# Performance work log

Measured on AMD Instinct MI355X. Metric: run time of the kernel, lower is better.

Reference implementation:

```python
import jax, jax.numpy as jnp
import numpy as np

N = 4096      # nodes (= attention seq_len)
D = 256       # dim_h
H = 4         # num_heads
HD = D // H   # head dim
E = 131072    # edges (avg degree 32)


def _ln(x, g, b, eps=1e-5):
    mu = jnp.mean(x, -1, keepdims=True)
    var = jnp.var(x, -1, keepdims=True)
    return (x - mu) * jax.lax.rsqrt(var + eps) * g + b


def setup_inputs() -> dict:
    key = jax.random.key(0)
    ks = jax.random.split(key, 10)
    s = 0.02
    nrm = lambda k, shape: jax.random.normal(k, shape, jnp.float32) * s
    return dict(
        x=jax.random.normal(ks[0], (N, D), jnp.float32),
        edge_index=jax.random.randint(ks[1], (2, E), 0, N, dtype=jnp.int32),
        W_gcn=nrm(ks[2], (D, D)), b_gcn=jnp.zeros((D,), jnp.float32),
        w_qkv=nrm(ks[3], (D, 3 * D)), b_qkv=jnp.zeros((3 * D,), jnp.float32),
        w_out=nrm(ks[4], (D, D)), b_out=jnp.zeros((D,), jnp.float32),
        g1l=jnp.ones((D,), jnp.float32), beta1l=jnp.zeros((D,), jnp.float32),
        g1a=jnp.ones((D,), jnp.float32), beta1a=jnp.zeros((D,), jnp.float32),
        W1=nrm(ks[5], (D, 2 * D)), bf1=jnp.zeros((2 * D,), jnp.float32),
        W2=nrm(ks[6], (2 * D, D)), bf2=jnp.zeros((D,), jnp.float32),
        g2=jnp.ones((D,), jnp.float32), beta2=jnp.zeros((D,), jnp.float32),
    )


def reference(x, edge_index, W_gcn, b_gcn, w_qkv, b_qkv, w_out, b_out,
              g1l, beta1l, g1a, beta1a, W1, bf1, W2, bf2, g2, beta2):
    n = x.shape[0]
    # --- GCNConv: sym-normalized aggregation with self loops ---
    loop = jnp.arange(n, dtype=edge_index.dtype)
    src = jnp.concatenate([edge_index[0], loop])
    dst = jnp.concatenate([edge_index[1], loop])
    deg = jax.ops.segment_sum(jnp.ones_like(src, x.dtype), dst, num_segments=n)
    dinv = jax.lax.rsqrt(deg)  # deg >= 1 thanks to self loops
    h = x @ W_gcn                                  # [N, D]
    msg = h[src] * (dinv[src] * dinv[dst])[:, None]  # gather + edge norm
    x_local = jax.ops.segment_sum(msg, dst, num_segments=n) + b_gcn
    x = _ln(x + x_local, g1l, beta1l)
    # --- Multi-head self-attention over all nodes (one sequence) ---
    qkv = x @ w_qkv + b_qkv
    q, k, v = jnp.split(qkv, 3, axis=-1)
    q = q.reshape(n, H, HD)
    k = k.reshape(n, H, HD)
    v = v.reshape(n, H, HD)
    scale = 1.0 / (HD ** 0.5)
    scores = jnp.einsum('nhd,mhd->hnm', q, k) * scale   # [H, N, N]
    attn = jax.nn.softmax(scores, axis=-1)
    x_attn = jnp.einsum('hnm,mhd->nhd', attn, v).reshape(n, D) @ w_out + b_out
    x = _ln(x + x_attn, g1a, beta1a)
    # --- FFN (D -> 2D -> D, ReLU) ---
    x_ffn = jax.nn.relu(x @ W1 + bf1) @ W2 + bf2
    return _ln(x + x_ffn, g2, beta2)
```

## Files before the change

### kernel.cpp

```cpp
#include <hip/hip_runtime.h>

typedef unsigned short u16;
typedef __bf16 bf16x8 __attribute__((ext_vector_type(8)));
typedef float f32x4 __attribute__((ext_vector_type(4)));

__device__ __forceinline__ u16 f2u(float f) {
    unsigned u = __builtin_bit_cast(unsigned, f);
    return (u16)((u + 0x7FFFu + ((u >> 16) & 1u)) >> 16);
}

__device__ __forceinline__ float u2f(u16 h) {
    return __builtin_bit_cast(float, (unsigned)h << 16);
}

__device__ __forceinline__ void glds16(const u16* g, u16* l) {
    __builtin_amdgcn_global_load_lds((const __attribute__((address_space(1))) unsigned int*)g,
                                     (__attribute__((address_space(3))) unsigned int*)l, 16, 0, 0);
}


__global__ __launch_bounds__(256) void prep_k(
    const float* __restrict__ w0, const float* __restrict__ w1, const float* __restrict__ w2,
    const float* __restrict__ w3, const float* __restrict__ w4, const float* __restrict__ x,
    u16* __restrict__ o0, u16* __restrict__ o1, u16* __restrict__ o2,
    u16* __restrict__ o3, u16* __restrict__ o4, u16* __restrict__ xo,
    int* __restrict__ cnt, int xblocks, int nn) {
    int b = blockIdx.x, t = threadIdx.x;
    if (b < 144) {
        const float* in; u16* out; int R, C, tb;
        if (b < 16)       { in = w0; out = o0; R = 256; C = 256; tb = b; }
        else if (b < 64)  { in = w1; out = o1; R = 256; C = 768; tb = b - 16; }
        else if (b < 80)  { in = w2; out = o2; R = 256; C = 256; tb = b - 64; }
        else if (b < 112) { in = w3; out = o3; R = 256; C = 512; tb = b - 80; }
        else              { in = w4; out = o4; R = 512; C = 256; tb = b - 112; }
        int tcols = C >> 6;
        int tr = tb / tcols, tc = tb - tr * tcols;
        __shared__ float T[64][65];
        int i0 = t >> 6, j = t & 63;
#pragma unroll
        for (int p = 0; p < 16; p++) {
            int r = p * 4 + i0;
            T[r][j] = in[(long)(tr * 64 + r) * C + tc * 64 + j];
        }
        __syncthreads();
#pragma unroll
        for (int p = 0; p < 16; p++) {
            int c = p * 4 + i0;
            out[(long)(tc * 64 + c) * R + tr * 64 + j] = f2u(T[j][c]);
        }
    } else if (b < 144 + xblocks) {
        long base = (long)(b - 144) * 4096;
#pragma unroll
        for (int p = 0; p < 4; p++) {
            long idx = base + p * 1024 + t * 4;
            float4 v = *(const float4*)&x[idx];
            unsigned lo = (unsigned)f2u(v.x) | ((unsigned)f2u(v.y) << 16);
            unsigned hi = (unsigned)f2u(v.z) | ((unsigned)f2u(v.w) << 16);
            *(uint2*)&xo[idx] = uint2{lo, hi};
        }
    } else {
        int i = (b - 144 - xblocks) * 256 + t;
        if (i < nn) cnt[i] = 0;
    }
}


__device__ __forceinline__ void block_ln_stats(float v, float& mu, float& rstd) {
    float s1 = v, s2 = v * v;
#pragma unroll
    for (int m = 1; m < 64; m <<= 1) { s1 += __shfl_xor(s1, m, 64); s2 += __shfl_xor(s2, m, 64); }
    __shared__ float r1[4], r2[4];
    int lane = threadIdx.x & 63, w = threadIdx.x >> 6;
    if (lane == 0) { r1[w] = s1; r2[w] = s2; }
    __syncthreads();
    s1 = r1[0] + r1[1] + r1[2] + r1[3];
    s2 = r2[0] + r2[1] + r2[2] + r2[3];
    mu = s1 * (1.0f / 256.0f);
    float var = s2 * (1.0f / 256.0f) - mu * mu;
    rstd = rsqrtf(var + 1e-5f);
}

__global__ __launch_bounds__(256) void ln_k(const float* __restrict__ a, const float* __restrict__ b,
                                            const float* __restrict__ g, const float* __restrict__ be,
                                            float* __restrict__ out, u16* __restrict__ outbf) {
    int n = blockIdx.x, d = threadIdx.x;
    long i = (long)n * 256 + d;
    float v = a[i] + b[i];
    float mu, rs;
    block_ln_stats(v, mu, rs);
    float y = (v - mu) * rs * g[d] + be[d];
    out[i] = y;
    if (outbf) outbf[i] = f2u(y);
}


__global__ __launch_bounds__(256) void gcn_agg_ln_k(
    const u16* __restrict__ h, const float* __restrict__ x,
    const int* __restrict__ srcs, const int* __restrict__ cnt,
    const float* __restrict__ bg,
    const float* __restrict__ g, const float* __restrict__ be,
    float* __restrict__ x1, u16* __restrict__ x1bf) {
    int n = blockIdx.x, d = threadIdx.x;
    int c = cnt[n]; c = c < 128 ? c : 128;
    int st = n << 7;
    float dn = rsqrtf((float)(c + 1));
    float agg = u2f(h[(long)n * 256 + d]) * dn;
    int e = 0;
    for (; e + 4 <= c; e += 4) {
        int s0 = srcs[st + e], s1 = srcs[st + e + 1], s2 = srcs[st + e + 2], s3 = srcs[st + e + 3];
        float a0 = u2f(h[(long)s0 * 256 + d]) * rsqrtf((float)(cnt[s0] + 1));
        float a1 = u2f(h[(long)s1 * 256 + d]) * rsqrtf((float)(cnt[s1] + 1));
        float a2 = u2f(h[(long)s2 * 256 + d]) * rsqrtf((float)(cnt[s2] + 1));
        float a3 = u2f(h[(long)s3 * 256 + d]) * rsqrtf((float)(cnt[s3] + 1));
        agg += (a0 + a1) + (a2 + a3);
    }
    for (; e < c; e++) {
        int s = srcs[st + e];
        agg += u2f(h[(long)s * 256 + d]) * rsqrtf((float)(cnt[s] + 1));
    }
    float v = x[(long)n * 256 + d] + dn * agg + bg[d];
    float mu, rs;
    block_ln_stats(v, mu, rs);
    float y = (v - mu) * rs * g[d] + be[d];
    x1[(long)n * 256 + d] = y;
    x1bf[(long)n * 256 + d] = f2u(y);
}


template <int EPI>
__device__ __forceinline__ void gemm_body(
    int bx, int by,
    const u16* __restrict__ A, const u16* __restrict__ Bt,
    const float* __restrict__ bias, void* __restrict__ outp,
    int M, int N, int K) {
    __shared__ __align__(16) u16 As[64 * 256];
    __shared__ __align__(16) u16 Bs[64 * 256];
    int tid = threadIdx.x;
    int lane = tid & 63, w = tid >> 6;
    int l15 = lane & 15, quad = lane >> 4, l7 = l15 & 7;
    int m0 = bx * 64, n0 = by * 64;
    int wm = (w >> 1) * 32, wn = (w & 1) * 32;
    f32x4 acc[2][2];
#pragma unroll
    for (int i = 0; i < 2; i++)
#pragma unroll
        for (int j = 0; j < 2; j++) acc[i][j] = f32x4{0.f, 0.f, 0.f, 0.f};

    int rA0 = (wm + l15) * 256, rA1 = (wm + 16 + l15) * 256;
    int rB0 = (wn + l15) * 256, rB1 = (wn + 16 + l15) * 256;

    for (int kb = 0; kb < K; kb += 256) {
        if (kb) __syncthreads();
#pragma unroll
        for (int i = 0; i < 8; i++) {
            int s = i * 256 + tid;
            int j = s >> 5, dch = s & 31;
            int c = dch ^ (j & 7);
            glds16(A + (long)(m0 + j) * K + kb + c * 8, &As[s * 8]);
            glds16(Bt + (long)(n0 + j) * K + kb + c * 8, &Bs[s * 8]);
        }
        __syncthreads();
#pragma unroll
        for (int step = 0; step < 8; step++) {
            int d8 = (((step << 2) + quad) ^ l7) << 3;
            bf16x8 af0 = *(const bf16x8*)&As[rA0 + d8];
            bf16x8 af1 = *(const bf16x8*)&As[rA1 + d8];
            bf16x8 bf0 = *(const bf16x8*)&Bs[rB0 + d8];
            bf16x8 bf1 = *(const bf16x8*)&Bs[rB1 + d8];
            acc[0][0] = __builtin_amdgcn_mfma_f32_16x16x32_bf16(af0, bf0, acc[0][0], 0, 0, 0);
            acc[0][1] = __builtin_amdgcn_mfma_f32_16x16x32_bf16(af0, bf1, acc[0][1], 0, 0, 0);
            acc[1][0] = __builtin_amdgcn_mfma_f32_16x16x32_bf16(af1, bf0, acc[1][0], 0, 0, 0);
            acc[1][1] = __builtin_amdgcn_mfma_f32_16x16x32_bf16(af1, bf1, acc[1][1], 0, 0, 0);
        }
    }

#pragma unroll
    for (int nf = 0; nf < 2; nf++) {
        int col = n0 + wn + nf * 16 + l15;
        float bv = bias ? bias[col] : 0.0f;
#pragma unroll
        for (int mf = 0; mf < 2; mf++) {
#pragma unroll
            for (int r = 0; r < 4; r++) {
                int row = m0 + wm + mf * 16 + quad * 4 + r;
                float v = acc[mf][nf][r] + bv;
                if (EPI == 0) {
                    ((float*)outp)[(long)row * N + col] = v;
                } else if (EPI == 1) {
                    u16* q = (u16*)outp;
                    u16* kk = q + (long)M * 256;
                    u16* vt = kk + (long)M * 256;
                    if (col < 256) {
                        q[(((col >> 6) * (long)M) + row) * 64 + (col & 63)] = f2u(v * 0.180336884f);
                    } else if (col < 512) {
                        int c = col - 256;
                        kk[(((c >> 6) * (long)M) + row) * 64 + (c & 63)] = f2u(v);
                    } else {
                        int c = col - 512;
                        vt[((c >> 6) * 64 + (c & 63)) * (long)M + row] = f2u(v);
                    }
                } else if (EPI == 2) {
                    ((u16*)outp)[(long)row * N + col] = f2u(v > 0.f ? v : 0.f);
                } else {
                    ((u16*)outp)[(long)row * N + col] = f2u(v);
                }
            }
        }
    }
}

template <int EPI>
__global__ __launch_bounds__(256) void gemm_k(
    const u16* __restrict__ A, const u16* __restrict__ Bt,
    const float* __restrict__ bias, void* __restrict__ outp,
    int M, int N, int K) {
    gemm_body<EPI>(blockIdx.x, blockIdx.y, A, Bt, bias, outp, M, N, K);
}


__global__ __launch_bounds__(256) void front_k(
    const int* __restrict__ ei, int E, int* __restrict__ cnt, int* __restrict__ srcs,
    const u16* __restrict__ A, const u16* __restrict__ Bt, void* __restrict__ outp,
    int M, int N, int K, int SB) {
    int b = blockIdx.x;
    if (b < SB) {
        int e = b * 256 + threadIdx.x;
        if (e < E) {
            int s = ei[e], d = ei[E + e];
            int p = atomicAdd(&cnt[d], 1);
            if (p < 128) srcs[(d << 7) + p] = s;
        }
    } else {
        int id = b - SB;
        gemm_body<3>(id & 63, id >> 6, A, Bt, nullptr, outp, M, N, K);
    }
}


__global__ __launch_bounds__(256) void attn_k(const u16* __restrict__ qg, const u16* __restrict__ kg,
                                              const u16* __restrict__ vtg, float* __restrict__ po,
                                              float* __restrict__ pl, int N, int S) {
    int tid = threadIdx.x;
    int w = tid >> 6, lane = tid & 63, l15 = lane & 15, quad = lane >> 4;
    int lid = blockIdx.x + 64 * blockIdx.y + 256 * blockIdx.z;
    int hs = lid & 15;
    int hh = hs & 3, sp = hs >> 2, qb = lid >> 4;
    int q0 = qb * 64 + w * 16;
    int kbeg = sp * (N / S);
    int nit = (N / S) / 64;
    const u16* qh = qg + (long)hh * N * 64;
    const u16* kh = kg + (long)hh * N * 64;
    const u16* vh = vtg + (long)hh * 64 * N;

    __shared__ __align__(16) u16 KV[2][2][4096];
    __shared__ __align__(16) u16 P[4][1024];
    u16* Pw = &P[w][0];

    int s0 = tid, j0 = s0 >> 3, c0s = ((s0 & 7) ^ (j0 & 7)) * 8;
    int s1 = tid + 256, j1 = s1 >> 3, c1s = ((s1 & 7) ^ (j1 & 7)) * 8;
    const u16* kp0 = kh + (long)(kbeg + j0) * 64 + c0s;
    const u16* kp1 = kh + (long)(kbeg + j1) * 64 + c1s;
    const u16* vp0 = vh + (long)j0 * N + kbeg + c0s;
    const u16* vp1 = vh + (long)j1 * N + kbeg + c1s;
    u16* lk0[2] = {&KV[0][0][s0 * 8], &KV[1][0][s0 * 8]};
    u16* lk1[2] = {&KV[0][0][s1 * 8], &KV[1][0][s1 * 8]};
    u16* lv0[2] = {&KV[0][1][s0 * 8], &KV[1][1][s0 * 8]};
    u16* lv1[2] = {&KV[0][1][s1 * 8], &KV[1][1][s1 * 8]};

    int lo3 = l15 & 7;
    int c0 = (quad ^ lo3) * 8;
    int c1 = c0 ^ 32;
    int ps = lo3 << 1;
    int pw0 = l15 * 64 + (((quad << 1) ^ ps) << 2);
    int pw1 = l15 * 64 + (((8 + (quad << 1)) ^ ps) << 2);
    int pca[4];
#pragma unroll
    for (int nt = 0; nt < 4; nt++) pca[nt] = l15 * 64 + (((nt * 4 + quad) ^ ps) << 2);

    bf16x8 aq0 = *(const bf16x8*)(qh + (long)(q0 + l15) * 64 + quad * 8);
    bf16x8 aq1 = *(const bf16x8*)(qh + (long)(q0 + l15) * 64 + 32 + quad * 8);
    bf16x8 ones;
#pragma unroll
    for (int i = 0; i < 8; i++) ones[i] = (__bf16)1.0f;

    f32x4 o[4];
#pragma unroll
    for (int dn = 0; dn < 4; dn++) o[dn] = f32x4{0.f, 0.f, 0.f, 0.f};
    f32x4 accl = f32x4{0.f, 0.f, 0.f, 0.f};

    glds16(kp0, lk0[0]); glds16(kp1, lk1[0]);
    glds16(vp0, lv0[0]); glds16(vp1, lv1[0]);
    kp0 += 4096; kp1 += 4096; vp0 += 64; vp1 += 64;

    for (int it = 0; it < nit; it++) {
        __syncthreads();
        if (it + 1 < nit) {
            int nb = (it + 1) & 1;
            glds16(kp0, lk0[nb]); glds16(kp1, lk1[nb]);
            glds16(vp0, lv0[nb]); glds16(vp1, lv1[nb]);
            kp0 += 4096; kp1 += 4096; vp0 += 64; vp1 += 64;
        }
        const u16* Kc = &KV[it & 1][0][0];
        const u16* Vc = &KV[it & 1][1][0];
#pragma unroll
        for (int nt = 0; nt < 4; nt++) {
            const u16* Kr = Kc + (nt * 16 + l15) * 64;
            bf16x8 kf0 = *(const bf16x8*)(Kr + c0);
            bf16x8 kf1 = *(const bf16x8*)(Kr + c1);
            f32x4 s = f32x4{0.f, 0.f, 0.f, 0.f};
            s = __builtin_amdgcn_mfma_f32_16x16x32_bf16(kf0, aq0, s, 0, 0, 0);
            s = __builtin_amdgcn_mfma_f32_16x16x32_bf16(kf1, aq1, s, 0, 0, 0);
            unsigned u0 = (unsigned)((int)(s[0] * 8388608.0f) + 1064992209);
            unsigned u1 = (unsigned)((int)(s[1] * 8388608.0f) + 1064992209);
            unsigned u2 = (unsigned)((int)(s[2] * 8388608.0f) + 1064992209);
            unsigned u3 = (unsigned)((int)(s[3] * 8388608.0f) + 1064992209);
            unsigned pk01 = __builtin_amdgcn_perm(u1, u0, 0x07060302u);
            unsigned pk23 = __builtin_amdgcn_perm(u3, u2, 0x07060302u);
            *(uint2*)&Pw[pca[nt]] = uint2{pk01, pk23};
        }
        bf16x8 pa0 = *(const bf16x8*)&Pw[pw0];
        bf16x8 pa1 = *(const bf16x8*)&Pw[pw1];
        accl = __builtin_amdgcn_mfma_f32_16x16x32_bf16(pa0, ones, accl, 0, 0, 0);
        accl = __builtin_amdgcn_mfma_f32_16x16x32_bf16(pa1, ones, accl, 0, 0, 0);
#pragma unroll
        for (int dn = 0; dn < 4; dn++) {
            const u16* Vr = Vc + (dn * 16 + l15) * 64;
            bf16x8 v0 = *(const bf16x8*)(Vr + c0);
            bf16x8 v1 = *(const bf16x8*)(Vr + c1);
            o[dn] = __builtin_amdgcn_mfma_f32_16x16x32_bf16(pa0, v0, o[dn], 0, 0, 0);
            o[dn] = __builtin_amdgcn_mfma_f32_16x16x32_bf16(pa1, v1, o[dn], 0, 0, 0);
        }
    }

    long pbase = ((long)(sp * 4 + hh)) * N;
#pragma unroll
    for (int dn = 0; dn < 4; dn++)
#pragma unroll
        for (int r = 0; r < 4; r++) {
            int row = q0 + quad * 4 + r;
            po[(pbase + row) * 64 + dn * 16 + l15] = o[dn][r];
        }
    if (l15 == 0) {
#pragma unroll
        for (int r = 0; r < 4; r++) pl[pbase + q0 + quad * 4 + r] = accl[r];
    }
}

__global__ __launch_bounds__(256) void attn_comb_k(const float* __restrict__ po, const float* __restrict__ pl,
                                                   u16* __restrict__ xo, int N, int S) {
    int n = blockIdx.x, c = threadIdx.x;
    int hh = c >> 6, d = c & 63;
    float osum = 0.f, lsum = 0.f;
    for (int s = 0; s < S; s++) {
        osum += po[(((long)(s * 4 + hh)) * N + n) * 64 + d];
        lsum += pl[((long)(s * 4 + hh)) * N + n];
    }
    xo[(long)n * 256 + c] = f2u(osum / lsum);
}


extern "C" void kernel_launch(void* const* d_in, const int* in_sizes, int n_in,
                              void* d_out, int out_size, void* d_ws, size_t ws_size,
                              hipStream_t stream) {
    const float* x    = (const float*)d_in[0];
    const int*   ei   = (const int*)d_in[1];
    const float* Wg   = (const float*)d_in[2];
    const float* bg   = (const float*)d_in[3];
    const float* Wqkv = (const float*)d_in[4];
    const float* bqkv = (const float*)d_in[5];
    const float* Wo   = (const float*)d_in[6];
    const float* bo   = (const float*)d_in[7];
    const float* g1l  = (const float*)d_in[8];
    const float* b1l  = (const float*)d_in[9];
    const float* g1a  = (const float*)d_in[10];
    const float* b1a  = (const float*)d_in[11];
    const float* W1   = (const float*)d_in[12];
    const float* bf1  = (const float*)d_in[13];
    const float* W2   = (const float*)d_in[14];
    const float* bf2  = (const float*)d_in[15];
    const float* g2   = (const float*)d_in[16];
    const float* b2   = (const float*)d_in[17];
    float* out = (float*)d_out;

    int N = in_sizes[0] / 256;
    int E = in_sizes[1] / 2;
    const int S = 4;

    char* p = (char*)d_ws;
    auto alloc = [&](size_t bytes) { void* r = (void*)p; p += (bytes + 255) & ~(size_t)255; return r; };
    u16*   wg_t   = (u16*)alloc((size_t)256 * 256 * 2);
    u16*   wqkv_t = (u16*)alloc((size_t)256 * 768 * 2);
    u16*   wo_t   = (u16*)alloc((size_t)256 * 256 * 2);
    u16*   w1_t   = (u16*)alloc((size_t)512 * 256 * 2);
    u16*   w2_t   = (u16*)alloc((size_t)256 * 512 * 2);
    u16*   xbf    = (u16*)alloc((size_t)N * 256 * 2);
    u16*   h      = (u16*)alloc((size_t)N * 256 * 2);
    int*   cnt    = (int*)alloc((size_t)N * 4);
    int*   srcs   = (int*)alloc((size_t)N * 128 * 4);
    float* x1     = (float*)alloc((size_t)N * 256 * 4);
    u16*   x1bf   = (u16*)alloc((size_t)N * 256 * 2);
    u16*   qkv    = (u16*)alloc((size_t)3 * N * 256 * 2);
    u16*   xattn  = (u16*)alloc((size_t)N * 256 * 2);
    float* attno  = (float*)alloc((size_t)N * 256 * 4);
    float* x2     = (float*)alloc((size_t)N * 256 * 4);
    u16*   x2bf   = (u16*)alloc((size_t)N * 256 * 2);
    u16*   ffn1   = (u16*)alloc((size_t)N * 512 * 2);
    float* ffno   = (float*)alloc((size_t)N * 256 * 4);
    float* po     = (float*)alloc((size_t)S * 4 * N * 64 * 4);
    float* pl     = (float*)alloc((size_t)S * 4 * N * 4);

    dim3 b256(256);

    int xblocks = (N * 256) / 4096;
    int cblocks = (N + 255) / 256;
    prep_k<<<144 + xblocks + cblocks, b256, 0, stream>>>(Wg, Wqkv, Wo, W1, W2, x,
                                                         wg_t, wqkv_t, wo_t, w1_t, w2_t, xbf,
                                                         cnt, xblocks, N);

    int SB = (E + 255) / 256;
    front_k<<<SB + (N / 64) * 4, b256, 0, stream>>>(ei, E, cnt, srcs, xbf, wg_t, h, N, 256, 256, SB);

    gcn_agg_ln_k<<<N, b256, 0, stream>>>(h, x, srcs, cnt, bg, g1l, b1l, x1, x1bf);

    gemm_k<1><<<dim3(N / 64, 12), b256, 0, stream>>>(x1bf, wqkv_t, bqkv, qkv, N, 768, 256);
    attn_k<<<dim3(N / 64, 4, S), b256, 0, stream>>>(qkv, qkv + (size_t)N * 256, qkv + (size_t)2 * N * 256,
                                                    po, pl, N, S);
    attn_comb_k<<<N, b256, 0, stream>>>(po, pl, xattn, N, S);
    gemm_k<0><<<dim3(N / 64, 4), b256, 0, stream>>>(xattn, wo_t, bo, attno, N, 256, 256);
    ln_k<<<N, b256, 0, stream>>>(x1, attno, g1a, b1a, x2, x2bf);

    gemm_k<2><<<dim3(N / 64, 8), b256, 0, stream>>>(x2bf, w1_t, bf1, ffn1, N, 512, 256);
    gemm_k<0><<<dim3(N / 64, 4), b256, 0, stream>>>(ffn1, w2_t, bf2, ffno, N, 256, 512);
    ln_k<<<N, b256, 0, stream>>>(x2, ffno, g2, b2, out, nullptr);
}
```

Measured before the change: 193.7 us.

## Fuse output projections with residual LayerNorm and halve attention key splits

```diff
diff --git a/kernel.cpp b/kernel.cpp
--- a/kernel.cpp
+++ b/kernel.cpp
@@ -78,19 +78,6 @@
     mu = s1 * (1.0f / 256.0f);
     float var = s2 * (1.0f / 256.0f) - mu * mu;
     rstd = rsqrtf(var + 1e-5f);
-}
-
-__global__ __launch_bounds__(256) void ln_k(const float* __restrict__ a, const float* __restrict__ b,
-                                            const float* __restrict__ g, const float* __restrict__ be,
-                                            float* __restrict__ out, u16* __restrict__ outbf) {
-    int n = blockIdx.x, d = threadIdx.x;
-    long i = (long)n * 256 + d;
-    float v = a[i] + b[i];
-    float mu, rs;
-    block_ln_stats(v, mu, rs);
-    float y = (v - mu) * rs * g[d] + be[d];
-    out[i] = y;
-    if (outbf) outbf[i] = f2u(y);
 }
 
 
@@ -184,9 +171,7 @@
             for (int r = 0; r < 4; r++) {
                 int row = m0 + wm + mf * 16 + quad * 4 + r;
                 float v = acc[mf][nf][r] + bv;
-                if (EPI == 0) {
-                    ((float*)outp)[(long)row * N + col] = v;
-                } else if (EPI == 1) {
+                if (EPI == 1) {
                     u16* q = (u16*)outp;
                     u16* kk = q + (long)M * 256;
                     u16* vt = kk + (long)M * 256;
@@ -218,6 +203,100 @@
 }
 
 
+template <int WRITE_BF>
+__global__ __launch_bounds__(256) void gemm_ln_k(
+    const u16* __restrict__ A, const u16* __restrict__ Bt, const float* __restrict__ bias,
+    const float* __restrict__ res, const float* __restrict__ g, const float* __restrict__ be,
+    float* __restrict__ outf, u16* __restrict__ outbf, int M, int K) {
+    __shared__ __align__(16) u16 As[16 * 64];
+    __shared__ __align__(16) u16 Bs[256 * 64];
+    __shared__ float red[2][4][16];
+    int tid = threadIdx.x;
+    int lane = tid & 63, w = tid >> 6;
+    int l15 = lane & 15, quad = lane >> 4, l7 = l15 & 7;
+    int m0 = blockIdx.x * 16;
+    f32x4 acc[4];
+#pragma unroll
+    for (int i = 0; i < 4; i++) acc[i] = f32x4{0.f, 0.f, 0.f, 0.f};
+
+    int jA = tid >> 3, dA = tid & 7, cA = dA ^ (jA & 7);
+    const u16* agp = A + (long)(m0 + jA) * K + cA * 8;
+
+    for (int kb = 0; kb < K; kb += 64) {
+        if (kb) __syncthreads();
+        if (tid < 128) glds16(agp + kb, &As[tid * 8]);
+#pragma unroll
+        for (int i = 0; i < 8; i++) {
+            int s = i * 256 + tid;
+            int jb = s >> 3, db = s & 7, cb = db ^ (jb & 7);
+            glds16(Bt + (long)jb * K + kb + cb * 8, &Bs[s * 8]);
+        }
+        __syncthreads();
+#pragma unroll
+        for (int step = 0; step < 2; step++) {
+            int d8 = (((step << 2) + quad) ^ l7) << 3;
+            bf16x8 af = *(const bf16x8*)&As[l15 * 64 + d8];
+#pragma unroll
+            for (int nf = 0; nf < 4; nf++) {
+                int rb = w * 64 + nf * 16 + l15;
+                bf16x8 bfr = *(const bf16x8*)&Bs[rb * 64 + d8];
+                acc[nf] = __builtin_amdgcn_mfma_f32_16x16x32_bf16(af, bfr, acc[nf], 0, 0, 0);
+            }
+        }
+    }
+
+    float vv[4][4];
+    float p1[4] = {0.f, 0.f, 0.f, 0.f}, p2[4] = {0.f, 0.f, 0.f, 0.f};
+#pragma unroll
+    for (int nf = 0; nf < 4; nf++) {
+        int col = w * 64 + nf * 16 + l15;
+        float bv = bias[col];
+#pragma unroll
+        for (int r = 0; r < 4; r++) {
+            int row = m0 + quad * 4 + r;
+            float v = acc[nf][r] + bv + res[(long)row * 256 + col];
+            vv[nf][r] = v;
+            p1[r] += v; p2[r] += v * v;
+        }
+    }
+#pragma unroll
+    for (int m = 1; m < 16; m <<= 1) {
+#pragma unroll
+        for (int r = 0; r < 4; r++) {
+            p1[r] += __shfl_xor(p1[r], m, 64);
+            p2[r] += __shfl_xor(p2[r], m, 64);
+        }
+    }
+    if (l15 == 0) {
+#pragma unroll
+        for (int r = 0; r < 4; r++) { red[0][w][quad * 4 + r] = p1[r]; red[1][w][quad * 4 + r] = p2[r]; }
+    }
+    __syncthreads();
+    float mu[4], rs[4];
+#pragma unroll
+    for (int r = 0; r < 4; r++) {
+        int rr = quad * 4 + r;
+        float s1 = red[0][0][rr] + red[0][1][rr] + red[0][2][rr] + red[0][3][rr];
+        float s2 = red[1][0][rr] + red[1][1][rr] + red[1][2][rr] + red[1][3][rr];
+        mu[r] = s1 * (1.0f / 256.0f);
+        float var = s2 * (1.0f / 256.0f) - mu[r] * mu[r];
+        rs[r] = rsqrtf(var + 1e-5f);
+    }
+#pragma unroll
+    for (int nf = 0; nf < 4; nf++) {
+        int col = w * 64 + nf * 16 + l15;
+        float gg = g[col], bb = be[col];
+#pragma unroll
+        for (int r = 0; r < 4; r++) {
+            int row = m0 + quad * 4 + r;
+            float y = (vv[nf][r] - mu[r]) * rs[r] * gg + bb;
+            outf[(long)row * 256 + col] = y;
+            if (WRITE_BF) outbf[(long)row * 256 + col] = f2u(y);
+        }
+    }
+}
+
+
 __global__ __launch_bounds__(256) void front_k(
     const int* __restrict__ ei, int E, int* __restrict__ cnt, int* __restrict__ srcs,
     const u16* __restrict__ A, const u16* __restrict__ Bt, void* __restrict__ outp,
@@ -243,8 +322,8 @@
     int tid = threadIdx.x;
     int w = tid >> 6, lane = tid & 63, l15 = lane & 15, quad = lane >> 4;
     int lid = blockIdx.x + 64 * blockIdx.y + 256 * blockIdx.z;
-    int hs = lid & 15;
-    int hh = hs & 3, sp = hs >> 2, qb = lid >> 4;
+    int hs = lid & 7;
+    int hh = hs & 3, sp = hs >> 2, qb = lid >> 3;
     int q0 = qb * 64 + w * 16;
     int kbeg = sp * (N / S);
     int nit = (N / S) / 64;
@@ -384,7 +463,7 @@
 
     int N = in_sizes[0] / 256;
     int E = in_sizes[1] / 2;
-    const int S = 4;
+    const int S = 2;
 
     char* p = (char*)d_ws;
     auto alloc = [&](size_t bytes) { void* r = (void*)p; p += (bytes + 255) & ~(size_t)255; return r; };
@@ -401,11 +480,9 @@
     u16*   x1bf   = (u16*)alloc((size_t)N * 256 * 2);
     u16*   qkv    = (u16*)alloc((size_t)3 * N * 256 * 2);
     u16*   xattn  = (u16*)alloc((size_t)N * 256 * 2);
-    float* attno  = (float*)alloc((size_t)N * 256 * 4);
     float* x2     = (float*)alloc((size_t)N * 256 * 4);
     u16*   x2bf   = (u16*)alloc((size_t)N * 256 * 2);
     u16*   ffn1   = (u16*)alloc((size_t)N * 512 * 2);
-    float* ffno   = (float*)alloc((size_t)N * 256 * 4);
     float* po     = (float*)alloc((size_t)S * 4 * N * 64 * 4);
     float* pl     = (float*)alloc((size_t)S * 4 * N * 4);
 
@@ -426,10 +503,10 @@
     attn_k<<<dim3(N / 64, 4, S), b256, 0, stream>>>(qkv, qkv + (size_t)N * 256, qkv + (size_t)2 * N * 256,
                                                     po, pl, N, S);
     attn_comb_k<<<N, b256, 0, stream>>>(po, pl, xattn, N, S);
-    gemm_k<0><<<dim3(N / 64, 4), b256, 0, stream>>>(xattn, wo_t, bo, attno, N, 256, 256);
-    ln_k<<<N, b256, 0, stream>>>(x1, attno, g1a, b1a, x2, x2bf);
+
+    gemm_ln_k<1><<<N / 16, b256, 0, stream>>>(xattn, wo_t, bo, x1, g1a, b1a, x2, x2bf, N, 256);
 
     gemm_k<2><<<dim3(N / 64, 8), b256, 0, stream>>>(x2bf, w1_t, bf1, ffn1, N, 512, 256);
-    gemm_k<0><<<dim3(N / 64, 4), b256, 0, stream>>>(ffn1, w2_t, bf2, ffno, N, 256, 512);
-    ln_k<<<N, b256, 0, stream>>>(x2, ffno, g2, b2, out, nullptr);
-}
+
+    gemm_ln_k<0><<<N / 16, b256, 0, stream>>>(ffn1, w2_t, bf2, x2, g2, b2, out, nullptr, N, 512);
+}
```

Result: no change. 195.0 us (+0.7%).
